# Performance work log

Measured on AMD Instinct MI355X. Metric: run time of the kernel, lower is better.

The kernel has to match this reference:

```python
import jax, jax.numpy as jnp
import numpy as np

EPS = 1e-5
HEADS, DK, DV = 8, 32, 64
SCALE = DK ** -0.5

def _bn(x, gamma, beta, mean, var):
    # eval-mode BatchNorm1d over channel dim of [b, c, n]
    inv = gamma / jnp.sqrt(var + EPS)
    return (x - mean[None, :, None]) * inv[None, :, None] + beta[None, :, None]

def setup_inputs() -> dict:
    key = jax.random.key(0)
    ks = jax.random.split(key, 24)
    dim, n, dim_out = 256, 1024, 256
    idk, idv = DK * HEADS, DV * HEADS
    def bn_params(k, c):
        k1, k2, k3, k4 = jax.random.split(k, 4)
        return (jax.random.normal(k1, (c,)) * 0.1 + 1.0,   # gamma
                jax.random.normal(k2, (c,)) * 0.1,          # beta
                jax.random.normal(k3, (c,)) * 0.1,          # running mean
                jax.random.uniform(k4, (c,)) * 0.5 + 0.5)   # running var > 0
    q_g, q_b, q_m, q_v = bn_params(ks[1], idk)
    k_g, k_b, k_m, k_v = bn_params(ks[2], idk)
    v_g, v_b, v_m, v_v = bn_params(ks[3], idv)
    o_g, o_b, o_m, o_v = bn_params(ks[4], dim_out)
    return {
        'x': jax.random.normal(ks[0], (8, dim, n), dtype=jnp.float32),
        'Wq': jax.random.normal(ks[5], (idk, dim)) * (dim ** -0.5),
        'Wk': jax.random.normal(ks[6], (idk, dim)) * (dim ** -0.5),
        'Wv': jax.random.normal(ks[7], (idv, dim)) * (dim ** -0.5),
        'Wo': jax.random.normal(ks[8], (dim_out, idv)) * (idv ** -0.5),
        'bo': jax.random.normal(ks[9], (dim_out,)) * 0.02,
        'pos_emb': jax.random.normal(ks[10], (n, HEADS)) * 0.02,
        'q_gamma': q_g, 'q_beta': q_b, 'q_mean': q_m, 'q_var': q_v,
        'k_gamma': k_g, 'k_beta': k_b, 'k_mean': k_m, 'k_var': k_v,
        'v_gamma': v_g, 'v_beta': v_b, 'v_mean': v_m, 'v_var': v_v,
        'o_gamma': o_g, 'o_beta': o_b, 'o_mean': o_m, 'o_var': o_v,
    }

def reference(x, Wq, Wk, Wv, Wo, bo, pos_emb,
              q_gamma, q_beta, q_mean, q_var,
              k_gamma, k_beta, k_mean, k_var,
              v_gamma, v_beta, v_mean, v_var,
              o_gamma, o_beta, o_mean, o_var):
    b, _, n = x.shape
    # 1x1 conv == channel matmul, then BN
    q = _bn(jnp.einsum('bcn,oc->bon', x, Wq), q_gamma, q_beta, q_mean, q_var)
    k = _bn(jnp.einsum('bcn,oc->bon', x, Wk), k_gamma, k_beta, k_mean, k_var)
    v = _bn(jnp.einsum('bcn,oc->bon', x, Wv), v_gamma, v_beta, v_mean, v_var)
    # b (h d) n -> b h n d
    q = q.reshape(b, HEADS, DK, n).transpose(0, 1, 3, 2)
    k = k.reshape(b, HEADS, DK, n).transpose(0, 1, 3, 2)
    v = v.reshape(b, HEADS, DV, n).transpose(0, 1, 3, 2)
    dots = jnp.einsum('bhid,bhjd->bhij', q, k) * SCALE
    # relative-position bias: emb[|i-j|] -> [n, n, h] -> [1, h, n, n]
    rel = jnp.abs(jnp.arange(n)[:, None] - jnp.arange(n)[None, :])
    bias = pos_emb[rel].transpose(2, 0, 1)[None]
    dots = dots + bias / SCALE
    attn = jax.nn.softmax(dots, axis=-1)
    out = jnp.einsum('bhij,bhjd->bhid', attn, v)
    # b h n d -> b (h d) n
    out = out.transpose(0, 1, 3, 2).reshape(b, HEADS * DV, n)
    out = jax.nn.gelu(out, approximate=False)
    out = jnp.einsum('bcn,oc->bon', out, Wo) + bo[None, :, None]
    return _bn(out, o_gamma, o_beta, o_mean, o_var)
```

## Files before the change

kernel.cpp:

```cpp
#include <hip/hip_runtime.h>
#include <hip/hip_bf16.h>

#define HEADS 8
#define DK 32
#define DV 64
#define DIM 256
#define NCTX 1024
#define NB 8
#define IDK 256
#define IDV 512
#define SCALE 0.17677669529663687f
#define INV_SCALE 5.656854249492381f
#define LOG2E 1.4426950408889634f
#define BN_EPS 1e-5f
#define THR 11.5416f

typedef __bf16 bf16x8 __attribute__((ext_vector_type(8)));
typedef __bf16 bf16x4 __attribute__((ext_vector_type(4)));
typedef float f32x4 __attribute__((ext_vector_type(4)));
typedef float f32x16 __attribute__((ext_vector_type(16)));

static __device__ __forceinline__ unsigned short bfbits(float v) {
  __bf16 b = (__bf16)v;
  return __builtin_bit_cast(unsigned short, b);
}

__global__ __launch_bounds__(256) void k_prep_trans(
    const float* __restrict__ x,
    const float* __restrict__ Wq, const float* __restrict__ Wk,
    const float* __restrict__ Wv, const float* __restrict__ Wo,
    const float* __restrict__ bo, const float* __restrict__ pe,
    const float* __restrict__ qg, const float* __restrict__ qb,
    const float* __restrict__ qm, const float* __restrict__ qv,
    const float* __restrict__ kg, const float* __restrict__ kb,
    const float* __restrict__ km, const float* __restrict__ kv,
    const float* __restrict__ vg, const float* __restrict__ vb,
    const float* __restrict__ vm, const float* __restrict__ vv,
    const float* __restrict__ og, const float* __restrict__ ob,
    const float* __restrict__ om, const float* __restrict__ ov,
    __bf16* __restrict__ xT, __bf16* __restrict__ WB, float* __restrict__ BB,
    uint2* __restrict__ Tq4g) {
  int bid = blockIdx.x;
  if (bid < 1605) {
    int idx = bid * 256 + threadIdx.x;
    if (idx < 65536) {
      int o = idx >> 8;
      WB[idx] = (__bf16)(Wq[idx] * (qg[o] * rsqrtf(qv[o] + BN_EPS) * SCALE * LOG2E));
    } else if (idx < 131072) {
      int i = idx - 65536, o = i >> 8;
      WB[idx] = (__bf16)(Wk[i] * (kg[o] * rsqrtf(kv[o] + BN_EPS)));
    } else if (idx < 262144) {
      int i = idx - 131072, o = i >> 8;
      WB[idx] = (__bf16)(Wv[i] * (vg[o] * rsqrtf(vv[o] + BN_EPS)));
    } else if (idx < 393216) {
      int i = idx - 262144, o = i >> 9;
      WB[idx] = (__bf16)(Wo[i] * (og[o] * rsqrtf(ov[o] + BN_EPS)));
    } else if (idx < 394496) {
      int i = idx - 393216;
      if (i < 256) {
        float sc = qg[i] * rsqrtf(qv[i] + BN_EPS);
        BB[i] = (qb[i] - qm[i] * sc) * SCALE * LOG2E;
      } else if (i < 512) {
        int o = i - 256;
        float sc = kg[o] * rsqrtf(kv[o] + BN_EPS);
        BB[i] = kb[o] - km[o] * sc;
      } else if (i < 1024) {
        int o = i - 512;
        float sc = vg[o] * rsqrtf(vv[o] + BN_EPS);
        BB[i] = vb[o] - vm[o] * sc;
      } else {
        int o = i - 1024;
        float sc = og[o] * rsqrtf(ov[o] + BN_EPS);
        BB[i] = (bo[o] - om[o]) * sc + ob[o];
      }
    } else {
      int i = idx - 394496;
      int h = i >> 11, t = i & 2047;
      unsigned short us[4];
#pragma unroll
      for (int rr = 0; rr < 4; ++rr) {
        int d = t - rr - 1023; d = d < 0 ? -d : d; d = d > 1023 ? 1023 : d;
        us[rr] = bfbits(pe[(size_t)d * HEADS + h] * INV_SCALE * LOG2E);
      }
      uint2 e;
      e.x = (unsigned)us[0] | ((unsigned)us[1] << 16);
      e.y = (unsigned)us[2] | ((unsigned)us[3] << 16);
      Tq4g[((size_t)h << 11) + t] = e;
    }
  } else {
    __shared__ float t[64][65];
    int tb = bid - 1605;
    int b = tb >> 6, c0 = ((tb >> 4) & 3) * 64, n0 = (tb & 15) * 64;
    int col = threadIdx.x & 63, rb = threadIdx.x >> 6;
    const float* xp = x + ((size_t)b * DIM + c0) * NCTX + n0;
#pragma unroll
    for (int r = 0; r < 16; ++r) {
      int row = rb + 4 * r;
      t[row][col] = xp[(size_t)row * NCTX + col];
    }
    __syncthreads();
    __bf16* op = xT + ((size_t)b * NCTX + n0) * DIM + c0;
#pragma unroll
    for (int r = 0; r < 16; ++r) {
      int i = rb + 4 * r;
      op[(size_t)i * DIM + col] = (__bf16)t[col][i];
    }
  }
}

__global__ __launch_bounds__(256, 2) void k_gemm_qkv(
    const __bf16* __restrict__ Xsrc, const __bf16* __restrict__ Wsrc,
    const float* __restrict__ Bias, __bf16* __restrict__ Qws,
    __bf16* __restrict__ Kws, __bf16* __restrict__ Vws) {
  int bx = blockIdx.x, by = blockIdx.y;
  int mode = by < 2 ? 0 : (by < 4 ? 1 : 2);
  int tid = threadIdx.x, wave = tid >> 6, lane = tid & 63;
  int wm = wave >> 1, wn = wave & 1;
  int l16 = lane & 15, g = (lane >> 4) & 3, g4 = g * 4;
  int R0 = bx * 128;

  __shared__ __align__(16) char XTl[16384];
  __shared__ __align__(16) char WTl[16384];

  int sr = tid >> 1, sh = tid & 1;
  const __bf16* xg = Xsrc + (size_t)(R0 + sr) * DIM + sh * 32;
  const __bf16* wg = Wsrc + (size_t)(by * 128 + sr) * DIM + sh * 32;
  int wbase = sr * 128;
  int gsw[4];
#pragma unroll
  for (int q = 0; q < 4; ++q) gsw[q] = ((sh * 4 + q) ^ (sr & 7)) * 16;

  bf16x8 sx[4], sw[4];
#pragma unroll
  for (int q = 0; q < 4; ++q) {
    sx[q] = *reinterpret_cast<const bf16x8*>(xg + q * 8);
    sw[q] = *reinterpret_cast<const bf16x8*>(wg + q * 8);
  }

  f32x4 acc[4][4] = {};
  const char* Abase = (mode <= 1) ? WTl : XTl;
  const char* Bbase = (mode <= 1) ? XTl : WTl;

  for (int st = 0; st < 4; ++st) {
    __syncthreads();
#pragma unroll
    for (int q = 0; q < 4; ++q) {
      *reinterpret_cast<bf16x8*>(XTl + wbase + gsw[q]) = sx[q];
      *reinterpret_cast<bf16x8*>(WTl + wbase + gsw[q]) = sw[q];
    }
    __syncthreads();
    if (st + 1 < 4) {
      const __bf16* xn = xg + (st + 1) * 64;
      const __bf16* wn_ = wg + (st + 1) * 64;
#pragma unroll
      for (int q = 0; q < 4; ++q) {
        sx[q] = *reinterpret_cast<const bf16x8*>(xn + q * 8);
        sw[q] = *reinterpret_cast<const bf16x8*>(wn_ + q * 8);
      }
    }
#pragma unroll
    for (int kc = 0; kc < 2; ++kc) {
      bf16x8 af[4], bf[4];
#pragma unroll
      for (int t = 0; t < 4; ++t) {
        int ra = wm * 64 + t * 16 + l16;
        af[t] = *reinterpret_cast<const bf16x8*>(
            Abase + ra * 128 + (((kc * 4 + g) ^ (ra & 7)) * 16));
        int rb = wn * 64 + t * 16 + l16;
        bf[t] = *reinterpret_cast<const bf16x8*>(
            Bbase + rb * 128 + (((kc * 4 + g) ^ (rb & 7)) * 16));
      }
      __builtin_amdgcn_s_setprio(1);
#pragma unroll
      for (int mt = 0; mt < 4; ++mt)
#pragma unroll
        for (int nt = 0; nt < 4; ++nt)
          acc[mt][nt] = __builtin_amdgcn_mfma_f32_16x16x32_bf16(
              af[mt], bf[nt], acc[mt][nt], 0, 0, 0);
      __builtin_amdgcn_s_setprio(0);
    }
  }

  if (mode <= 1) {
    __bf16* OWS = (mode == 0) ? Qws : Kws;
    const float* bb = Bias + (mode == 0 ? 0 : 256);
    int oq0 = by * 128 - (mode == 1 ? 256 : 0) + wm * 64;
#pragma unroll
    for (int mt = 0; mt < 4; ++mt) {
      int oq = oq0 + mt * 16 + g4;
      float4 b4 = *reinterpret_cast<const float4*>(&bb[oq]);
      int h = oq >> 5, d0 = oq & 31;
#pragma unroll
      for (int nt = 0; nt < 4; ++nt) {
        int i = R0 + wn * 64 + nt * 16 + l16;
        int b = i >> 10, n = i & 1023;
        bf16x4 pk;
        pk[0] = (__bf16)(acc[mt][nt][0] + b4.x);
        pk[1] = (__bf16)(acc[mt][nt][1] + b4.y);
        pk[2] = (__bf16)(acc[mt][nt][2] + b4.z);
        pk[3] = (__bf16)(acc[mt][nt][3] + b4.w);
        *reinterpret_cast<bf16x4*>(
            &OWS[(((size_t)b * HEADS + h) * NCTX + n) * DK + d0]) = pk;
      }
    }
  } else {
#pragma unroll
    for (int nt = 0; nt < 4; ++nt) {
      int vo = (by - 4) * 128 + wn * 64 + nt * 16 + l16;
      float bia = Bias[512 + vo];
#pragma unroll
      for (int mt = 0; mt < 4; ++mt) {
        int i0 = R0 + wm * 64 + mt * 16 + g4;
        int b = i0 >> 10, n = i0 & 1023;
        bf16x4 pk;
#pragma unroll
        for (int rr = 0; rr < 4; ++rr) pk[rr] = (__bf16)(acc[mt][nt][rr] + bia);
        *reinterpret_cast<bf16x4*>(&Vws[((size_t)b * IDV + vo) * NCTX + n]) = pk;
      }
    }
  }
}

__global__ __launch_bounds__(256, 2) void k_gemm_out(
    const __bf16* __restrict__ G, const __bf16* __restrict__ WoB,
    const float* __restrict__ bo2, float* __restrict__ out) {
  int bx = blockIdx.x, by = blockIdx.y;
  int tid = threadIdx.x, wave = tid >> 6, lane = tid & 63;
  int wm = wave >> 1, wn = wave & 1;
  int l16 = lane & 15, g = (lane >> 4) & 3, g4 = g * 4;
  int R0 = bx * 128;

  __shared__ __align__(16) char XTl[16384];
  __shared__ __align__(16) char WTl[8192];

  int sr = tid >> 1, sh = tid & 1;
  const __bf16* xg = G + (size_t)(R0 + sr) * IDV + sh * 32;
  int xbase = sr * 128;
  int gsw[4];
#pragma unroll
  for (int q = 0; q < 4; ++q) gsw[q] = ((sh * 4 + q) ^ (sr & 7)) * 16;

  int wsr = tid >> 2, wq = tid & 3;
  const __bf16* wg = WoB + (size_t)(by * 64 + wsr) * IDV + wq * 16;
  int wbase = wsr * 128;
  int gswW[2];
#pragma unroll
  for (int q = 0; q < 2; ++q) gswW[q] = ((wq * 2 + q) ^ (wsr & 7)) * 16;

  bf16x8 sx[4], sw[2];
#pragma unroll
  for (int q = 0; q < 4; ++q) sx[q] = *reinterpret_cast<const bf16x8*>(xg + q * 8);
#pragma unroll
  for (int q = 0; q < 2; ++q) sw[q] = *reinterpret_cast<const bf16x8*>(wg + q * 8);

  f32x4 acc[4][2] = {};

  for (int st = 0; st < 8; ++st) {
    __syncthreads();
#pragma unroll
    for (int q = 0; q < 4; ++q) *reinterpret_cast<bf16x8*>(XTl + xbase + gsw[q]) = sx[q];
#pragma unroll
    for (int q = 0; q < 2; ++q) *reinterpret_cast<bf16x8*>(WTl + wbase + gswW[q]) = sw[q];
    __syncthreads();
    if (st + 1 < 8) {
      const __bf16* xn = xg + (st + 1) * 64;
      const __bf16* wn_ = wg + (st + 1) * 64;
#pragma unroll
      for (int q = 0; q < 4; ++q) sx[q] = *reinterpret_cast<const bf16x8*>(xn + q * 8);
#pragma unroll
      for (int q = 0; q < 2; ++q) sw[q] = *reinterpret_cast<const bf16x8*>(wn_ + q * 8);
    }
#pragma unroll
    for (int kc = 0; kc < 2; ++kc) {
      bf16x8 af[4], bf[2];
#pragma unroll
      for (int t = 0; t < 4; ++t) {
        int ra = wm * 64 + t * 16 + l16;
        af[t] = *reinterpret_cast<const bf16x8*>(
            XTl + ra * 128 + (((kc * 4 + g) ^ (ra & 7)) * 16));
      }
#pragma unroll
      for (int t = 0; t < 2; ++t) {
        int rb = wn * 32 + t * 16 + l16;
        bf[t] = *reinterpret_cast<const bf16x8*>(
            WTl + rb * 128 + (((kc * 4 + g) ^ (rb & 7)) * 16));
      }
      __builtin_amdgcn_s_setprio(1);
#pragma unroll
      for (int mt = 0; mt < 4; ++mt)
#pragma unroll
        for (int nt = 0; nt < 2; ++nt)
          acc[mt][nt] = __builtin_amdgcn_mfma_f32_16x16x32_bf16(
              af[mt], bf[nt], acc[mt][nt], 0, 0, 0);
      __builtin_amdgcn_s_setprio(0);
    }
  }
#pragma unroll
  for (int nt = 0; nt < 2; ++nt) {
    int o = by * 64 + wn * 32 + nt * 16 + l16;
    float bia = bo2[o];
#pragma unroll
    for (int mt = 0; mt < 4; ++mt) {
      int i0 = R0 + wm * 64 + mt * 16 + g4;
      int b = i0 >> 10, n = i0 & 1023;
      float4 st;
      st.x = acc[mt][nt][0] + bia;
      st.y = acc[mt][nt][1] + bia;
      st.z = acc[mt][nt][2] + bia;
      st.w = acc[mt][nt][3] + bia;
      *reinterpret_cast<float4*>(&out[((size_t)b * DIM + o) * NCTX + n]) = st;
    }
  }
}

__global__ __launch_bounds__(128, 3) void k_attn(
    const __bf16* __restrict__ Qws, const __bf16* __restrict__ Kws,
    const __bf16* __restrict__ Vws, const uint2* __restrict__ Tq4g,
    __bf16* __restrict__ G) {
  int flat = blockIdx.x;
  int swz = (flat & 7) * 128 + (flat >> 3);
  int iblk = swz & 15, bh = swz >> 4;
  int b = bh >> 3, h = bh & 7;
  int tid = threadIdx.x, wave = tid >> 6, lane = tid & 63;
  int l31 = lane & 31, hi = lane >> 5;

  __shared__ __align__(16) __bf16 Klds[64][40];
  __shared__ __align__(16) __bf16 Vlds[64 * 64];
  __shared__ __align__(16) uint2 TqL[1088];

  int i0b = iblk * 64;
  {
    const uint4* tg4 = reinterpret_cast<const uint4*>(Tq4g + ((size_t)h << 11) + i0b);
    uint4* tl4 = reinterpret_cast<uint4*>(TqL);
    for (int c = tid; c < 544; c += 128) tl4[c] = tg4[c];
  }

  int i0w = i0b + wave * 32;
  int irow = i0w + l31;
  const __bf16* qbase = Qws + (size_t)bh * NCTX * DK;
  const __bf16* kbase = Kws + (size_t)bh * NCTX * DK;
  const __bf16* vbase = Vws + ((size_t)b * IDV + h * DV) * NCTX;
  bf16x8 qf0 = *reinterpret_cast<const bf16x8*>(qbase + (size_t)irow * DK + 8 * hi);
  bf16x8 qf1 = *reinterpret_cast<const bf16x8*>(qbase + (size_t)irow * DK + 16 + 8 * hi);

  int r_ = tid >> 1, s2 = (tid & 1) * 2;
  const __bf16* kgp = kbase + (size_t)r_ * DK + 8 * s2;
  const __bf16* vgp = vbase + (size_t)r_ * NCTX + 8 * s2;
  __bf16* kw0 = &Klds[r_][8 * s2];
  __bf16* kw1 = &Klds[r_][8 * (s2 + 1)];
  __bf16* vw0 = Vlds + r_ * 64 + 8 * ((s2) ^ (r_ & 7));
  __bf16* vw1 = Vlds + r_ * 64 + 8 * ((s2 + 1) ^ (r_ & 7));
  __bf16* vw2 = Vlds + r_ * 64 + 8 * ((s2 + 4) ^ (r_ & 7));
  __bf16* vw3 = Vlds + r_ * 64 + 8 * ((s2 + 5) ^ (r_ & 7));

  bf16x8 rk0 = *reinterpret_cast<const bf16x8*>(kgp);
  bf16x8 rk1 = *reinterpret_cast<const bf16x8*>(kgp + 8);
  bf16x8 rv0 = *reinterpret_cast<const bf16x8*>(vgp);
  bf16x8 rv1 = *reinterpret_cast<const bf16x8*>(vgp + 8);
  bf16x8 rv2 = *reinterpret_cast<const bf16x8*>(vgp + 32);
  bf16x8 rv3 = *reinterpret_cast<const bf16x8*>(vgp + 40);

  f32x16 acc0 = {}, acc1 = {};
  float m = -1e30f, s = 0.0f;
  int kxb = wave * 32 + l31 + 1023 - 4 * hi;
  const bf16x4* Tqp = reinterpret_cast<const bf16x4*>(TqL);

  for (int it = 0; it < 16; ++it) {
    int j0 = it * 64;
    __syncthreads();
    *reinterpret_cast<bf16x8*>(kw0) = rk0;
    *reinterpret_cast<bf16x8*>(kw1) = rk1;
    *reinterpret_cast<bf16x8*>(vw0) = rv0;
    *reinterpret_cast<bf16x8*>(vw1) = rv1;
    *reinterpret_cast<bf16x8*>(vw2) = rv2;
    *reinterpret_cast<bf16x8*>(vw3) = rv3;
    __syncthreads();
    int jn = (j0 + 64) & (NCTX - 1);
    rk0 = *reinterpret_cast<const bf16x8*>(kgp + (size_t)jn * DK);
    rk1 = *reinterpret_cast<const bf16x8*>(kgp + (size_t)jn * DK + 8);
    rv0 = *reinterpret_cast<const bf16x8*>(vgp + jn);
    rv1 = *reinterpret_cast<const bf16x8*>(vgp + jn + 8);
    rv2 = *reinterpret_cast<const bf16x8*>(vgp + jn + 32);
    rv3 = *reinterpret_cast<const bf16x8*>(vgp + jn + 40);

    float sv[32];
#pragma unroll
    for (int jg = 0; jg < 2; ++jg) {
      bf16x8 kf0 = *reinterpret_cast<const bf16x8*>(&Klds[32 * jg + l31][8 * hi]);
      bf16x8 kf1 = *reinterpret_cast<const bf16x8*>(&Klds[32 * jg + l31][16 + 8 * hi]);
      f32x16 S = {};
      __builtin_amdgcn_s_setprio(1);
      S = __builtin_amdgcn_mfma_f32_32x32x16_bf16(kf0, qf0, S, 0, 0, 0);
      S = __builtin_amdgcn_mfma_f32_32x32x16_bf16(kf1, qf1, S, 0, 0, 0);
      __builtin_amdgcn_s_setprio(0);
      int kb_ = kxb - j0 - 32 * jg;
#pragma unroll
      for (int q = 0; q < 4; ++q) {
        bf16x4 q4 = Tqp[kb_ - 8 * q];
#pragma unroll
        for (int rr = 0; rr < 4; ++rr)
          sv[jg * 16 + q * 4 + rr] = S[q * 4 + rr] + (float)q4[rr];
      }
    }
    float pmax = sv[0];
#pragma unroll
    for (int k = 1; k < 32; ++k) pmax = fmaxf(pmax, sv[k]);
    if (__any(pmax > m + THR)) {
      float mx = fmaxf(pmax, __shfl_xor(pmax, 32));
      float mnew = fmaxf(m, mx);
      float corr = __builtin_amdgcn_exp2f(m - mnew);
      s *= corr; m = mnew;
#pragma unroll
      for (int r = 0; r < 16; ++r) {
        float cv = __shfl(corr, (r & 3) + 8 * (r >> 2) + 4 * hi);
        acc0[r] *= cv; acc1[r] *= cv;
      }
    }
#pragma unroll
    for (int k = 0; k < 32; ++k) sv[k] = __builtin_amdgcn_exp2f(sv[k] - m);
    float ps = 0.0f;
#pragma unroll
    for (int k = 0; k < 32; ++k) ps += sv[k];
    s += ps;
#pragma unroll
    for (int jg = 0; jg < 2; ++jg) {
#pragma unroll
      for (int u = 0; u < 2; ++u) {
        int base = jg * 16 + 8 * u;
        unsigned we0, we1, wo0, wo1;
        asm("v_cvt_pk_bf16_f32 %0, %1, %2" : "=v"(we0) : "v"(sv[base + 0]), "v"(sv[base + 1]));
        asm("v_cvt_pk_bf16_f32 %0, %1, %2" : "=v"(we1) : "v"(sv[base + 2]), "v"(sv[base + 3]));
        asm("v_cvt_pk_bf16_f32 %0, %1, %2" : "=v"(wo0) : "v"(sv[base + 4]), "v"(sv[base + 5]));
        asm("v_cvt_pk_bf16_f32 %0, %1, %2" : "=v"(wo1) : "v"(sv[base + 6]), "v"(sv[base + 7]));
        asm volatile("v_permlane32_swap_b32 %0, %1" : "+v"(we0), "+v"(wo0));
        asm volatile("v_permlane32_swap_b32 %0, %1" : "+v"(we1), "+v"(wo1));
        uint4 pw = {we0, we1, wo0, wo1};
        bf16x8 pfrag = *reinterpret_cast<bf16x8*>(&pw);
        int c = jg * 2 + u;
        int sl = 2 * c + hi;
        bf16x8 vf0 = *reinterpret_cast<const bf16x8*>(Vlds + l31 * 64 + 8 * (sl ^ (l31 & 7)));
        bf16x8 vf1 = *reinterpret_cast<const bf16x8*>(Vlds + (32 + l31) * 64 + 8 * (sl ^ (l31 & 7)));
        __builtin_amdgcn_s_setprio(1);
        acc0 = __builtin_amdgcn_mfma_f32_32x32x16_bf16(pfrag, vf0, acc0, 0, 0, 0);
        acc1 = __builtin_amdgcn_mfma_f32_32x32x16_bf16(pfrag, vf1, acc1, 0, 0, 0);
        __builtin_amdgcn_s_setprio(0);
      }
    }
  }
  float srow = s + __shfl_xor(s, 32);
  float inv = 1.0f / srow;
  __bf16* gbase = G + (size_t)b * NCTX * IDV + h * DV + l31;
#pragma unroll
  for (int r = 0; r < 16; ++r) {
    int il = (r & 3) + 8 * (r >> 2) + 4 * hi;
    float iv = __shfl(inv, il);
    float v0 = acc0[r] * iv, v1 = acc1[r] * iv;
    float g0 = 0.5f * v0 * (1.0f + erff(v0 * 0.70710678118654752f));
    float g1 = 0.5f * v1 * (1.0f + erff(v1 * 0.70710678118654752f));
    gbase[(size_t)(i0w + il) * IDV] = (__bf16)g0;
    gbase[(size_t)(i0w + il) * IDV + 32] = (__bf16)g1;
  }
}

extern "C" void kernel_launch(void* const* d_in, const int* in_sizes, int n_in,
                              void* d_out, int out_size, void* d_ws, size_t ws_size,
                              hipStream_t stream) {
  const float* x  = (const float*)d_in[0];
  const float* Wq = (const float*)d_in[1];
  const float* Wk = (const float*)d_in[2];
  const float* Wv = (const float*)d_in[3];
  const float* Wo = (const float*)d_in[4];
  const float* bo = (const float*)d_in[5];
  const float* pe = (const float*)d_in[6];
  const float* qg = (const float*)d_in[7];
  const float* qb = (const float*)d_in[8];
  const float* qm = (const float*)d_in[9];
  const float* qv = (const float*)d_in[10];
  const float* kg = (const float*)d_in[11];
  const float* kb = (const float*)d_in[12];
  const float* km = (const float*)d_in[13];
  const float* kv = (const float*)d_in[14];
  const float* vg = (const float*)d_in[15];
  const float* vb = (const float*)d_in[16];
  const float* vm = (const float*)d_in[17];
  const float* vv = (const float*)d_in[18];
  const float* og = (const float*)d_in[19];
  const float* ob = (const float*)d_in[20];
  const float* om = (const float*)d_in[21];
  const float* ov = (const float*)d_in[22];

  char* ws = (char*)d_ws;
  __bf16* xT = (__bf16*)(ws);
  __bf16* Q  = (__bf16*)(ws + (4ull << 20));
  __bf16* K  = (__bf16*)(ws + (8ull << 20));
  __bf16* V  = (__bf16*)(ws + (12ull << 20));
  __bf16* G  = (__bf16*)(ws + (20ull << 20));
  __bf16* WB = (__bf16*)(ws + (28ull << 20));
  float*  BB = (float*)(ws + (28ull << 20) + (768ull << 10));
  uint2*  Tq = (uint2*)(ws + (29ull << 20));
  float* out = (float*)d_out;

  k_prep_trans<<<dim3(2117), 256, 0, stream>>>(
      x, Wq, Wk, Wv, Wo, bo, pe, qg, qb, qm, qv, kg, kb, km, kv,
      vg, vb, vm, vv, og, ob, om, ov, xT, WB, BB, Tq);
  k_gemm_qkv<<<dim3(64, 8), 256, 0, stream>>>(xT, WB, BB, Q, K, V);
  k_attn<<<dim3(1024), 128, 0, stream>>>(Q, K, V, Tq, G);
  k_gemm_out<<<dim3(64, 4), 256, 0, stream>>>(G, WB + 262144, BB + 1024, out);
}
```

Before: 60.64 us.

## Load K/V MFMA fragments directly from global memory instead of LDS staging

Removes the shared-memory staging of K and V tiles, the register prefetch and the two barriers per iteration in the attention kernel. Each wave now loads its K and V MFMA operands straight from global memory, relying on the caches for reuse between the two waves. The launch bounds drop from 3 to 2 blocks per SM, which gives the compiler more registers. The cost is that the loads are no longer prefetched a tile ahead, so global latency is exposed inside the loop, and the duplicated loads across waves add cache traffic.

```diff
diff --git a/kernel.cpp b/kernel.cpp
--- a/kernel.cpp
+++ b/kernel.cpp
@@ -313,7 +313,7 @@
   }
 }
 
-__global__ __launch_bounds__(128, 3) void k_attn(
+__global__ __launch_bounds__(128, 2) void k_attn(
     const __bf16* __restrict__ Qws, const __bf16* __restrict__ Kws,
     const __bf16* __restrict__ Vws, const uint2* __restrict__ Tq4g,
     __bf16* __restrict__ G) {
@@ -324,8 +324,6 @@
   int tid = threadIdx.x, wave = tid >> 6, lane = tid & 63;
   int l31 = lane & 31, hi = lane >> 5;
 
-  __shared__ __align__(16) __bf16 Klds[64][40];
-  __shared__ __align__(16) __bf16 Vlds[64 * 64];
   __shared__ __align__(16) uint2 TqL[1088];
 
   int i0b = iblk * 64;
@@ -334,6 +332,7 @@
     uint4* tl4 = reinterpret_cast<uint4*>(TqL);
     for (int c = tid; c < 544; c += 128) tl4[c] = tg4[c];
   }
+  __syncthreads();
 
   int i0w = i0b + wave * 32;
   int irow = i0w + l31;
@@ -343,23 +342,6 @@
   bf16x8 qf0 = *reinterpret_cast<const bf16x8*>(qbase + (size_t)irow * DK + 8 * hi);
   bf16x8 qf1 = *reinterpret_cast<const bf16x8*>(qbase + (size_t)irow * DK + 16 + 8 * hi);
 
-  int r_ = tid >> 1, s2 = (tid & 1) * 2;
-  const __bf16* kgp = kbase + (size_t)r_ * DK + 8 * s2;
-  const __bf16* vgp = vbase + (size_t)r_ * NCTX + 8 * s2;
-  __bf16* kw0 = &Klds[r_][8 * s2];
-  __bf16* kw1 = &Klds[r_][8 * (s2 + 1)];
-  __bf16* vw0 = Vlds + r_ * 64 + 8 * ((s2) ^ (r_ & 7));
-  __bf16* vw1 = Vlds + r_ * 64 + 8 * ((s2 + 1) ^ (r_ & 7));
-  __bf16* vw2 = Vlds + r_ * 64 + 8 * ((s2 + 4) ^ (r_ & 7));
-  __bf16* vw3 = Vlds + r_ * 64 + 8 * ((s2 + 5) ^ (r_ & 7));
-
-  bf16x8 rk0 = *reinterpret_cast<const bf16x8*>(kgp);
-  bf16x8 rk1 = *reinterpret_cast<const bf16x8*>(kgp + 8);
-  bf16x8 rv0 = *reinterpret_cast<const bf16x8*>(vgp);
-  bf16x8 rv1 = *reinterpret_cast<const bf16x8*>(vgp + 8);
-  bf16x8 rv2 = *reinterpret_cast<const bf16x8*>(vgp + 32);
-  bf16x8 rv3 = *reinterpret_cast<const bf16x8*>(vgp + 40);
-
   f32x16 acc0 = {}, acc1 = {};
   float m = -1e30f, s = 0.0f;
   int kxb = wave * 32 + l31 + 1023 - 4 * hi;
@@ -367,27 +349,12 @@
 
   for (int it = 0; it < 16; ++it) {
     int j0 = it * 64;
-    __syncthreads();
-    *reinterpret_cast<bf16x8*>(kw0) = rk0;
-    *reinterpret_cast<bf16x8*>(kw1) = rk1;
-    *reinterpret_cast<bf16x8*>(vw0) = rv0;
-    *reinterpret_cast<bf16x8*>(vw1) = rv1;
-    *reinterpret_cast<bf16x8*>(vw2) = rv2;
-    *reinterpret_cast<bf16x8*>(vw3) = rv3;
-    __syncthreads();
-    int jn = (j0 + 64) & (NCTX - 1);
-    rk0 = *reinterpret_cast<const bf16x8*>(kgp + (size_t)jn * DK);
-    rk1 = *reinterpret_cast<const bf16x8*>(kgp + (size_t)jn * DK + 8);
-    rv0 = *reinterpret_cast<const bf16x8*>(vgp + jn);
-    rv1 = *reinterpret_cast<const bf16x8*>(vgp + jn + 8);
-    rv2 = *reinterpret_cast<const bf16x8*>(vgp + jn + 32);
-    rv3 = *reinterpret_cast<const bf16x8*>(vgp + jn + 40);
-
     float sv[32];
 #pragma unroll
     for (int jg = 0; jg < 2; ++jg) {
-      bf16x8 kf0 = *reinterpret_cast<const bf16x8*>(&Klds[32 * jg + l31][8 * hi]);
-      bf16x8 kf1 = *reinterpret_cast<const bf16x8*>(&Klds[32 * jg + l31][16 + 8 * hi]);
+      const __bf16* kr = kbase + (size_t)(j0 + 32 * jg + l31) * DK + 8 * hi;
+      bf16x8 kf0 = *reinterpret_cast<const bf16x8*>(kr);
+      bf16x8 kf1 = *reinterpret_cast<const bf16x8*>(kr + 16);
       f32x16 S = {};
       __builtin_amdgcn_s_setprio(1);
       S = __builtin_amdgcn_mfma_f32_32x32x16_bf16(kf0, qf0, S, 0, 0, 0);
@@ -436,10 +403,10 @@
         asm volatile("v_permlane32_swap_b32 %0, %1" : "+v"(we1), "+v"(wo1));
         uint4 pw = {we0, we1, wo0, wo1};
         bf16x8 pfrag = *reinterpret_cast<bf16x8*>(&pw);
-        int c = jg * 2 + u;
-        int sl = 2 * c + hi;
-        bf16x8 vf0 = *reinterpret_cast<const bf16x8*>(Vlds + l31 * 64 + 8 * (sl ^ (l31 & 7)));
-        bf16x8 vf1 = *reinterpret_cast<const bf16x8*>(Vlds + (32 + l31) * 64 + 8 * (sl ^ (l31 & 7)));
+        int sl = 2 * (jg * 2 + u) + hi;
+        const __bf16* vr = vbase + (size_t)l31 * NCTX + j0 + 8 * sl;
+        bf16x8 vf0 = *reinterpret_cast<const bf16x8*>(vr);
+        bf16x8 vf1 = *reinterpret_cast<const bf16x8*>(vr + 32 * NCTX);
         __builtin_amdgcn_s_setprio(1);
         acc0 = __builtin_amdgcn_mfma_f32_32x32x16_bf16(pfrag, vf0, acc0, 0, 0, 0);
         acc1 = __builtin_amdgcn_mfma_f32_32x32x16_bf16(pfrag, vf1, acc1, 0, 0, 0);
```

After: 75.38 us. +24.3%, slower.
